# Optimization experiments

Measured on AMD Instinct MI355X. Metric: run time of the kernel, lower is better.

Reference implementation:

```python
import jax, jax.numpy as jnp
import numpy as np

N = 100000

def _gcn_conv(x, W, b, row, col, norm, n_nodes):
    # x: [N, Fin], W: [Fin, Fout]; message = norm * (x W)[row], aggregated at col
    h = x @ W                                  # small GEMM
    msg = h[row] * norm[:, None]               # [E+N, Fout] gather (memory bound)
    out = jax.ops.segment_sum(msg, col, num_segments=n_nodes)
    return out + b

def _norm_coeffs(edge_index, n_nodes):
    # add self-loops, compute symmetric normalization deg^-1/2[row]*deg^-1/2[col]
    loops = jnp.arange(n_nodes, dtype=edge_index.dtype)
    row = jnp.concatenate([edge_index[0], loops])
    col = jnp.concatenate([edge_index[1], loops])
    deg = jax.ops.segment_sum(jnp.ones_like(col, dtype=jnp.float32), col,
                              num_segments=n_nodes)
    dinv = jnp.where(deg > 0, jax.lax.rsqrt(deg), 0.0)
    norm = dinv[row] * dinv[col]
    return row, col, norm

def setup_inputs() -> dict:
    key = jax.random.key(0)
    ks = jax.random.split(key, 4)
    x = jax.random.normal(ks[0], (N, 64), dtype=jnp.float32)
    edge_index = jax.random.randint(ks[1], (2, 1600000), 0, N, dtype=jnp.int64)
    W1 = jax.random.normal(ks[2], (64, 64), dtype=jnp.float32) / np.sqrt(64)
    b1 = jnp.zeros((64,), dtype=jnp.float32)
    W2 = jax.random.normal(ks[3], (64, 64), dtype=jnp.float32) / np.sqrt(64)
    b2 = jnp.zeros((64,), dtype=jnp.float32)
    return {"x": x, "edge_index": edge_index, "W1": W1, "b1": b1, "W2": W2, "b2": b2}

def reference(x, edge_index, W1, b1, W2, b2):
    row, col, norm = _norm_coeffs(edge_index, N)
    h = jax.nn.relu(_gcn_conv(x, W1, b1, row, col, norm, N))
    return _gcn_conv(h, W2, b2, row, col, norm, N)
```

## Files before the change

### kernel.cpp

```cpp
#include <hip/hip_runtime.h>


#define NPB 32
#define BSH 8
#define BSZ 256
#define PTILE 4096
#define CAP 6144
#define PADALLOW 3856
#define CROW (CAP + PADALLOW)

typedef __attribute__((ext_vector_type(8))) short bf16x8;
typedef __attribute__((ext_vector_type(4))) float f32x4;

__device__ __forceinline__ unsigned bf16_rne(float f) {
    unsigned b = __float_as_uint(f);
    return (b + 0x7fffu + ((b >> 16) & 1u)) >> 16;
}
__device__ __forceinline__ float bf16_lo(unsigned u) { return __uint_as_float(u << 16); }
__device__ __forceinline__ float bf16_hi(unsigned u) { return __uint_as_float(u & 0xffff0000u); }

__global__ __launch_bounds__(512) void k_count(const int* __restrict__ coli,
                                               int E, int N, int NB, int numTiles,
                                               int* __restrict__ tcnt) {
    __shared__ int hist[512];
    int t = threadIdx.x;
    int T = E + N;
    int tile = blockIdx.x;
    int tstart = tile * PTILE;
    int m = min(PTILE, T - tstart);
    for (int b = t; b < NB; b += 512) hist[b] = 0;
    __syncthreads();
    for (int i = t; i < m; i += 512) {
        int g = tstart + i;
        int c = (g < E) ? coli[g] : (g - E);
        atomicAdd(&hist[c >> BSH], 1);
    }
    __syncthreads();
    for (int b = t; b < NB; b += 512) tcnt[(size_t)tile * NB + b] = hist[b];
}

__global__ __launch_bounds__(512) void k_scan(int* __restrict__ tcnt,
                                              int* __restrict__ btot,
                                              int NB, int numTiles) {
    __shared__ int wsum[8];
    int b = blockIdx.x;
    int t = threadIdx.x;
    int lane = t & 63, wid = t >> 6;
    int base = 0;
    for (int c0 = 0; c0 < numTiles; c0 += 512) {
        int tt = c0 + t;
        int v = (tt < numTiles) ? tcnt[(size_t)tt * NB + b] : 0;
        int inc = v;
        #pragma unroll
        for (int d = 1; d < 64; d <<= 1) {
            int o = __shfl_up(inc, d);
            if (lane >= d) inc += o;
        }
        if (lane == 63) wsum[wid] = inc;
        __syncthreads();
        int woff = 0, ctot = 0;
        #pragma unroll
        for (int i = 0; i < 8; i++) {
            int s = wsum[i];
            if (i < wid) woff += s;
            ctot += s;
        }
        if (tt < numTiles) tcnt[(size_t)tt * NB + b] = b * CAP + base + woff + inc - v;
        base += ctot;
        __syncthreads();
    }
    if (t == 0) btot[b] = base;
}

__global__ __launch_bounds__(512) void k_scatter(const int* __restrict__ rowi,
                                                 const int* __restrict__ coli,
                                                 int E, int N, int NB, int numTiles,
                                                 const int* __restrict__ tcnt,
                                                 unsigned* __restrict__ pairs) {
    __shared__ int hist[512];
    __shared__ int lbase[512];
    __shared__ int gbase[512];
    __shared__ unsigned sorted[PTILE];
    __shared__ unsigned short sbkt[PTILE];
    __shared__ int wsum[8];
    int t = threadIdx.x;
    int T = E + N;
    int tile = blockIdx.x;
    int tstart = tile * PTILE;
    int m = min(PTILE, T - tstart);
    for (int b = t; b < NB; b += 512) {
        hist[b] = 0;
        gbase[b] = tcnt[(size_t)tile * NB + b];
    }
    __syncthreads();
    int c_reg[8];
    #pragma unroll
    for (int k = 0; k < 8; k++) {
        int i = t + k * 512;
        int c = 0;
        if (i < m) {
            int g = tstart + i;
            c = (g < E) ? coli[g] : (g - E);
            atomicAdd(&hist[c >> BSH], 1);
        }
        c_reg[k] = c;
    }
    __syncthreads();
    {
        int lane = t & 63, wid = t >> 6;
        int v = (t < NB) ? hist[t] : 0;
        int inc = v;
        #pragma unroll
        for (int d = 1; d < 64; d <<= 1) {
            int o = __shfl_up(inc, d);
            if (lane >= d) inc += o;
        }
        if (lane == 63) wsum[wid] = inc;
        __syncthreads();
        int woff = 0;
        for (int i = 0; i < wid; i++) woff += wsum[i];
        if (t < NB) lbase[t] = woff + inc - v;
        __syncthreads();
    }
    for (int b = t; b < NB; b += 512) hist[b] = 0;
    __syncthreads();
    #pragma unroll
    for (int k = 0; k < 8; k++) {
        int i = t + k * 512;
        if (i < m) {
            int g = tstart + i;
            int c = c_reg[k];
            int r = (g < E) ? rowi[g] : c;
            int b = c >> BSH;
            int lr = atomicAdd(&hist[b], 1);
            int pos = lbase[b] + lr;
            sorted[pos] = (unsigned)r | ((unsigned)(c & (BSZ - 1)) << 24);
            sbkt[pos] = (unsigned short)b;
        }
    }
    __syncthreads();
    for (int j = t; j < m; j += 512) {
        int b = sbkt[j];
        pairs[gbase[b] + (j - lbase[b])] = sorted[j];
    }
}

__global__ __launch_bounds__(1024) void k_bfill(const unsigned* __restrict__ pairs,
                                                const int* __restrict__ btot,
                                                int N,
                                                int* __restrict__ offsets,
                                                int* __restrict__ cnt,
                                                float* __restrict__ dinv,
                                                int* __restrict__ csrc) {
    __shared__ int scnt[BSZ];
    __shared__ int scur[BSZ];
    __shared__ int wsum[4];
    __shared__ int scsrc[CROW];
    int b = blockIdx.x;
    int t = threadIdx.x;
    int ebeg = b * CAP;
    int m = btot[b];
    int pbase = b * CROW;
    if (t < BSZ) scnt[t] = 0;
    __syncthreads();
    for (int i = t; i < m; i += 1024) {
        atomicAdd(&scnt[pairs[ebeg + i] >> 24], 1);
    }
    __syncthreads();
    int cval = 0, pc = 0, inc = 0;
    int lane = t & 63, wid = t >> 6;
    if (t < BSZ) {
        cval = scnt[t];
        pc = (cval + 15) & ~15;
        inc = pc;
        #pragma unroll
        for (int d = 1; d < 64; d <<= 1) {
            int o = __shfl_up(inc, d);
            if (lane >= d) inc += o;
        }
        if (lane == 63) wsum[wid] = inc;
    }
    __syncthreads();
    if (t < BSZ) {
        int woff = 0;
        for (int i = 0; i < wid; i++) woff += wsum[i];
        int offl = woff + inc - pc;
        int v = (b << BSH) + t;
        if (v < N) {
            offsets[v] = pbase + offl;
            cnt[v] = (cval + 1) & ~1;
            dinv[v] = rsqrtf((float)cval);
        }
        scur[t] = offl;
        for (int i = offl + cval; i < offl + pc; i++) scsrc[i] = N;
    }
    __syncthreads();
    for (int i = t; i < m; i += 1024) {
        unsigned pk = pairs[ebeg + i];
        int slot = atomicAdd(&scur[pk >> 24], 1);
        scsrc[slot] = (int)(pk & 0xFFFFFFu);
    }
    __syncthreads();
    int tot = wsum[0] + wsum[1] + wsum[2] + wsum[3];
    for (int j = t; j < tot; j += 1024) csrc[pbase + j] = scsrc[j];
}

template <bool BF16IN>
__global__ __launch_bounds__(256) void k_gemm(const void* __restrict__ Xv,
                                              const float* __restrict__ W,
                                              const float* __restrict__ dinv,
                                              unsigned* __restrict__ Hout,
                                              int N, int nSlabs, int slabStride) {
    __shared__ float SMEM[4224];
    int t = threadIdx.x;
    int lane = t & 63, w = t >> 6;
    int nn = lane & 15, kq = lane >> 4;

    for (int i = t; i < 1024; i += 256) ((float4*)SMEM)[i] = ((const float4*)W)[i];
    __syncthreads();
    bf16x8 Bf[2][4];
    #pragma unroll
    for (int kt = 0; kt < 2; kt++) {
        #pragma unroll
        for (int ct = 0; ct < 4; ct++) {
            union { bf16x8 v; unsigned short s[8]; } u;
            #pragma unroll
            for (int j = 0; j < 8; j++) {
                int k = kt * 32 + kq * 8 + j;
                u.s[j] = (unsigned short)bf16_rne(SMEM[k * 64 + ct * 16 + nn]);
            }
            Bf[kt][ct] = u.v;
        }
    }
    __syncthreads();

    float* outT = SMEM + w * 1056;

    for (int slab = blockIdx.x * 4 + w; slab < nSlabs; slab += slabStride) {
        int row0 = slab * 16;
        int rowA = min(row0 + nn, N - 1);
        bf16x8 A0, A1;
        if (BF16IN) {
            const uint4* X = (const uint4*)Xv;
            union { uint4 u; bf16x8 v; } a0, a1;
            a0.u = X[(size_t)rowA * 8 + kq];
            a1.u = X[(size_t)rowA * 8 + 4 + kq];
            A0 = a0.v; A1 = a1.v;
        } else {
            const float4* X = (const float4*)Xv;
            float4 f0 = X[(size_t)rowA * 16 + kq * 2];
            float4 f1 = X[(size_t)rowA * 16 + kq * 2 + 1];
            float4 f2 = X[(size_t)rowA * 16 + 8 + kq * 2];
            float4 f3 = X[(size_t)rowA * 16 + 8 + kq * 2 + 1];
            union { bf16x8 v; unsigned short s[8]; } a0, a1;
            a0.s[0] = (unsigned short)bf16_rne(f0.x); a0.s[1] = (unsigned short)bf16_rne(f0.y);
            a0.s[2] = (unsigned short)bf16_rne(f0.z); a0.s[3] = (unsigned short)bf16_rne(f0.w);
            a0.s[4] = (unsigned short)bf16_rne(f1.x); a0.s[5] = (unsigned short)bf16_rne(f1.y);
            a0.s[6] = (unsigned short)bf16_rne(f1.z); a0.s[7] = (unsigned short)bf16_rne(f1.w);
            a1.s[0] = (unsigned short)bf16_rne(f2.x); a1.s[1] = (unsigned short)bf16_rne(f2.y);
            a1.s[2] = (unsigned short)bf16_rne(f2.z); a1.s[3] = (unsigned short)bf16_rne(f2.w);
            a1.s[4] = (unsigned short)bf16_rne(f3.x); a1.s[5] = (unsigned short)bf16_rne(f3.y);
            a1.s[6] = (unsigned short)bf16_rne(f3.z); a1.s[7] = (unsigned short)bf16_rne(f3.w);
            A0 = a0.v; A1 = a1.v;
        }
        float dvm = dinv[rowA];

        f32x4 acc[4];
        #pragma unroll
        for (int ct = 0; ct < 4; ct++) acc[ct] = (f32x4){0.f, 0.f, 0.f, 0.f};
        #pragma unroll
        for (int ct = 0; ct < 4; ct++) {
            acc[ct] = __builtin_amdgcn_mfma_f32_16x16x32_bf16(A0, Bf[0][ct], acc[ct], 0, 0, 0);
            acc[ct] = __builtin_amdgcn_mfma_f32_16x16x32_bf16(A1, Bf[1][ct], acc[ct], 0, 0, 0);
        }

        #pragma unroll
        for (int reg = 0; reg < 4; reg++) {
            int r = kq * 4 + reg;
            float dv = __shfl(dvm, r);
            #pragma unroll
            for (int ct = 0; ct < 4; ct++) {
                outT[r * 66 + ct * 16 + nn] = acc[ct][reg] * dv;
            }
        }
        int rr = lane >> 2;
        int c0 = (lane & 3) * 16;
        int orow = row0 + rr;
        if (orow < N) {
            unsigned pk[8];
            #pragma unroll
            for (int i = 0; i < 8; i++) {
                float lo = outT[rr * 66 + c0 + 2 * i];
                float hi = outT[rr * 66 + c0 + 2 * i + 1];
                pk[i] = bf16_rne(lo) | (bf16_rne(hi) << 16);
            }
            uint4* dst = (uint4*)Hout + (size_t)orow * 8 + (lane & 3) * 2;
            dst[0] = make_uint4(pk[0], pk[1], pk[2], pk[3]);
            dst[1] = make_uint4(pk[4], pk[5], pk[6], pk[7]);
        } else if (orow == N) {
            uint4* dst = (uint4*)Hout + (size_t)N * 8 + (lane & 3) * 2;
            dst[0] = make_uint4(0, 0, 0, 0);
            dst[1] = make_uint4(0, 0, 0, 0);
        }
    }
}

template <bool RELU_BF16OUT>
__global__ __launch_bounds__(256) void k_agg(const uint4* __restrict__ H,
                                             const int* __restrict__ offsets,
                                             const int* __restrict__ cnt,
                                             const int* __restrict__ csrc,
                                             const float* __restrict__ dinv,
                                             const float* __restrict__ bias,
                                             void* __restrict__ outv, int N) {
    int t = threadIdx.x;
    int fl = t & 7;
    int v = blockIdx.x * NPB + (t >> 3);
    if (v >= N) return;
    int beg = offsets[v];
    int deg = cnt[v];
    const int2* cs2 = (const int2*)(csrc + beg);
    const char* hb = (const char*)H + ((unsigned)fl << 4);

    float a0 = 0.f, a1 = 0.f, a2 = 0.f, a3 = 0.f;
    float a4 = 0.f, a5 = 0.f, a6 = 0.f, a7 = 0.f;

#define ACC8(R) do {                                                        \
        uint4 dd = *(const uint4*)(hb + ((unsigned)(R) << 7));              \
        a0 += bf16_lo(dd.x); a1 += bf16_hi(dd.x);                           \
        a2 += bf16_lo(dd.y); a3 += bf16_hi(dd.y);                           \
        a4 += bf16_lo(dd.z); a5 += bf16_hi(dd.z);                           \
        a6 += bf16_lo(dd.w); a7 += bf16_hi(dd.w);                           \
    } while (0)

    int2 ss = cs2[0];
    for (int j = 2; j < deg; j += 2) {
        int2 nx = cs2[j >> 1];
        ACC8(ss.x);
        ACC8(ss.y);
        ss = nx;
    }
    ACC8(ss.x);
    ACC8(ss.y);
#undef ACC8

    float dv = dinv[v];
    const float4* b4 = (const float4*)bias;
    float4 bA = b4[fl * 2];
    float4 bB = b4[fl * 2 + 1];
    float r0 = fmaf(dv, a0, bA.x);
    float r1 = fmaf(dv, a1, bA.y);
    float r2 = fmaf(dv, a2, bA.z);
    float r3 = fmaf(dv, a3, bA.w);
    float r4 = fmaf(dv, a4, bB.x);
    float r5 = fmaf(dv, a5, bB.y);
    float r6 = fmaf(dv, a6, bB.z);
    float r7 = fmaf(dv, a7, bB.w);
    if (RELU_BF16OUT) {
        r0 = fmaxf(r0, 0.f); r1 = fmaxf(r1, 0.f);
        r2 = fmaxf(r2, 0.f); r3 = fmaxf(r3, 0.f);
        r4 = fmaxf(r4, 0.f); r5 = fmaxf(r5, 0.f);
        r6 = fmaxf(r6, 0.f); r7 = fmaxf(r7, 0.f);
        uint4 pk;
        pk.x = bf16_rne(r0) | (bf16_rne(r1) << 16);
        pk.y = bf16_rne(r2) | (bf16_rne(r3) << 16);
        pk.z = bf16_rne(r4) | (bf16_rne(r5) << 16);
        pk.w = bf16_rne(r6) | (bf16_rne(r7) << 16);
        ((uint4*)outv)[(size_t)v * 8 + fl] = pk;
    } else {
        float4* o = (float4*)outv + (size_t)v * 16 + fl * 2;
        o[0] = make_float4(r0, r1, r2, r3);
        o[1] = make_float4(r4, r5, r6, r7);
    }
}

extern "C" void kernel_launch(void* const* d_in, const int* in_sizes, int n_in,
                              void* d_out, int out_size, void* d_ws, size_t ws_size,
                              hipStream_t stream) {
    const float* x  = (const float*)d_in[0];
    const int*   ei = (const int*)d_in[1];
    const float* W1 = (const float*)d_in[2];
    const float* b1 = (const float*)d_in[3];
    const float* W2 = (const float*)d_in[4];
    const float* b2 = (const float*)d_in[5];
    float* out      = (float*)d_out;

    const int N = in_sizes[0] / 64;
    const int E = in_sizes[1] / 2;
    const int* row = ei;
    const int* col = ei + E;
    const int T = E + N;
    const int NB = (N + BSZ - 1) >> BSH;
    const int numTiles = (T + PTILE - 1) / PTILE;

    char* p = (char*)d_ws;
    auto alloc = [&](size_t bytes) { void* r = (void*)p; p += (bytes + 255) & ~(size_t)255; return r; };
    int*      tcnt    = (int*)alloc((size_t)NB * numTiles * 4);
    int*      btot    = (int*)alloc((size_t)(NB + 1) * 4);
    int*      offsets = (int*)alloc((size_t)N * 4);
    int*      cnt     = (int*)alloc((size_t)N * 4);
    float*    dinv    = (float*)alloc((size_t)N * 4);
    unsigned* pairs   = (unsigned*)alloc((size_t)NB * CAP * 4);
    int*      csrc    = (int*)alloc(((size_t)NB * CROW + 64) * 4);
    unsigned* hbuf    = (unsigned*)alloc((size_t)(N + 16) * 32 * 4);
    unsigned* abuf    = (unsigned*)alloc((size_t)(N + 16) * 32 * 4);

    k_count<<<numTiles, 512, 0, stream>>>(col, E, N, NB, numTiles, tcnt);
    k_scan<<<NB, 512, 0, stream>>>(tcnt, btot, NB, numTiles);
    k_scatter<<<numTiles, 512, 0, stream>>>(row, col, E, N, NB, numTiles, tcnt, pairs);
    k_bfill<<<NB, 1024, 0, stream>>>(pairs, btot, N, offsets, cnt, dinv, csrc);

    const int nSlabs = (N + 16) / 16;
    const int GEMM_BLOCKS = 1024;
    const int SLAB_STRIDE = GEMM_BLOCKS * 4;
    const int GB = (N + NPB - 1) / NPB;

    k_gemm<false><<<GEMM_BLOCKS, 256, 0, stream>>>(x, W1, dinv, hbuf, N, nSlabs, SLAB_STRIDE);
    k_agg<true><<<GB, 256, 0, stream>>>((const uint4*)hbuf, offsets, cnt, csrc, dinv, b1, abuf, N);
    k_gemm<true><<<GEMM_BLOCKS, 256, 0, stream>>>(abuf, W2, dinv, hbuf, N, nSlabs, SLAB_STRIDE);
    k_agg<false><<<GB, 256, 0, stream>>>((const uint4*)hbuf, offsets, cnt, csrc, dinv, b2, out, N);
}
```

Before: 198.0 us.

## Fuse first GEMM into count kernel and apply source dinv during aggregation

Takes the dinv source scaling out of the GEMM epilogue, so the first-layer GEMM no longer waits for degree computation. That GEMM now runs as extra blocks inside the edge-count kernel, overlapping with the histogram pass and removing one launch. In exchange, the aggregation loop gathers dinv[src] per edge and uses FMAs, adding extra scattered loads on the memory-bound gather path. The GEMM is also executed with 512-thread blocks within the fused launch.

```diff
diff --git a/kernel.cpp b/kernel.cpp
--- a/kernel.cpp
+++ b/kernel.cpp
@@ -8,6 +8,7 @@
 #define CAP 6144
 #define PADALLOW 3856
 #define CROW (CAP + PADALLOW)
+#define GEMMB 1024
 
 typedef __attribute__((ext_vector_type(8))) short bf16x8;
 typedef __attribute__((ext_vector_type(4))) float f32x4;
@@ -19,204 +20,18 @@
 __device__ __forceinline__ float bf16_lo(unsigned u) { return __uint_as_float(u << 16); }
 __device__ __forceinline__ float bf16_hi(unsigned u) { return __uint_as_float(u & 0xffff0000u); }
 
-__global__ __launch_bounds__(512) void k_count(const int* __restrict__ coli,
-                                               int E, int N, int NB, int numTiles,
-                                               int* __restrict__ tcnt) {
-    __shared__ int hist[512];
-    int t = threadIdx.x;
-    int T = E + N;
-    int tile = blockIdx.x;
-    int tstart = tile * PTILE;
-    int m = min(PTILE, T - tstart);
-    for (int b = t; b < NB; b += 512) hist[b] = 0;
-    __syncthreads();
-    for (int i = t; i < m; i += 512) {
-        int g = tstart + i;
-        int c = (g < E) ? coli[g] : (g - E);
-        atomicAdd(&hist[c >> BSH], 1);
-    }
-    __syncthreads();
-    for (int b = t; b < NB; b += 512) tcnt[(size_t)tile * NB + b] = hist[b];
-}
-
-__global__ __launch_bounds__(512) void k_scan(int* __restrict__ tcnt,
-                                              int* __restrict__ btot,
-                                              int NB, int numTiles) {
-    __shared__ int wsum[8];
-    int b = blockIdx.x;
-    int t = threadIdx.x;
-    int lane = t & 63, wid = t >> 6;
-    int base = 0;
-    for (int c0 = 0; c0 < numTiles; c0 += 512) {
-        int tt = c0 + t;
-        int v = (tt < numTiles) ? tcnt[(size_t)tt * NB + b] : 0;
-        int inc = v;
-        #pragma unroll
-        for (int d = 1; d < 64; d <<= 1) {
-            int o = __shfl_up(inc, d);
-            if (lane >= d) inc += o;
-        }
-        if (lane == 63) wsum[wid] = inc;
-        __syncthreads();
-        int woff = 0, ctot = 0;
-        #pragma unroll
-        for (int i = 0; i < 8; i++) {
-            int s = wsum[i];
-            if (i < wid) woff += s;
-            ctot += s;
-        }
-        if (tt < numTiles) tcnt[(size_t)tt * NB + b] = b * CAP + base + woff + inc - v;
-        base += ctot;
-        __syncthreads();
-    }
-    if (t == 0) btot[b] = base;
-}
-
-__global__ __launch_bounds__(512) void k_scatter(const int* __restrict__ rowi,
-                                                 const int* __restrict__ coli,
-                                                 int E, int N, int NB, int numTiles,
-                                                 const int* __restrict__ tcnt,
-                                                 unsigned* __restrict__ pairs) {
-    __shared__ int hist[512];
-    __shared__ int lbase[512];
-    __shared__ int gbase[512];
-    __shared__ unsigned sorted[PTILE];
-    __shared__ unsigned short sbkt[PTILE];
-    __shared__ int wsum[8];
-    int t = threadIdx.x;
-    int T = E + N;
-    int tile = blockIdx.x;
-    int tstart = tile * PTILE;
-    int m = min(PTILE, T - tstart);
-    for (int b = t; b < NB; b += 512) {
-        hist[b] = 0;
-        gbase[b] = tcnt[(size_t)tile * NB + b];
-    }
-    __syncthreads();
-    int c_reg[8];
-    #pragma unroll
-    for (int k = 0; k < 8; k++) {
-        int i = t + k * 512;
-        int c = 0;
-        if (i < m) {
-            int g = tstart + i;
-            c = (g < E) ? coli[g] : (g - E);
-            atomicAdd(&hist[c >> BSH], 1);
-        }
-        c_reg[k] = c;
-    }
-    __syncthreads();
-    {
-        int lane = t & 63, wid = t >> 6;
-        int v = (t < NB) ? hist[t] : 0;
-        int inc = v;
-        #pragma unroll
-        for (int d = 1; d < 64; d <<= 1) {
-            int o = __shfl_up(inc, d);
-            if (lane >= d) inc += o;
-        }
-        if (lane == 63) wsum[wid] = inc;
-        __syncthreads();
-        int woff = 0;
-        for (int i = 0; i < wid; i++) woff += wsum[i];
-        if (t < NB) lbase[t] = woff + inc - v;
-        __syncthreads();
-    }
-    for (int b = t; b < NB; b += 512) hist[b] = 0;
-    __syncthreads();
-    #pragma unroll
-    for (int k = 0; k < 8; k++) {
-        int i = t + k * 512;
-        if (i < m) {
-            int g = tstart + i;
-            int c = c_reg[k];
-            int r = (g < E) ? rowi[g] : c;
-            int b = c >> BSH;
-            int lr = atomicAdd(&hist[b], 1);
-            int pos = lbase[b] + lr;
-            sorted[pos] = (unsigned)r | ((unsigned)(c & (BSZ - 1)) << 24);
-            sbkt[pos] = (unsigned short)b;
-        }
-    }
-    __syncthreads();
-    for (int j = t; j < m; j += 512) {
-        int b = sbkt[j];
-        pairs[gbase[b] + (j - lbase[b])] = sorted[j];
-    }
-}
-
-__global__ __launch_bounds__(1024) void k_bfill(const unsigned* __restrict__ pairs,
-                                                const int* __restrict__ btot,
-                                                int N,
-                                                int* __restrict__ offsets,
-                                                int* __restrict__ cnt,
-                                                float* __restrict__ dinv,
-                                                int* __restrict__ csrc) {
-    __shared__ int scnt[BSZ];
-    __shared__ int scur[BSZ];
-    __shared__ int wsum[4];
-    __shared__ int scsrc[CROW];
-    int b = blockIdx.x;
-    int t = threadIdx.x;
-    int ebeg = b * CAP;
-    int m = btot[b];
-    int pbase = b * CROW;
-    if (t < BSZ) scnt[t] = 0;
-    __syncthreads();
-    for (int i = t; i < m; i += 1024) {
-        atomicAdd(&scnt[pairs[ebeg + i] >> 24], 1);
-    }
-    __syncthreads();
-    int cval = 0, pc = 0, inc = 0;
-    int lane = t & 63, wid = t >> 6;
-    if (t < BSZ) {
-        cval = scnt[t];
-        pc = (cval + 15) & ~15;
-        inc = pc;
-        #pragma unroll
-        for (int d = 1; d < 64; d <<= 1) {
-            int o = __shfl_up(inc, d);
-            if (lane >= d) inc += o;
-        }
-        if (lane == 63) wsum[wid] = inc;
-    }
-    __syncthreads();
-    if (t < BSZ) {
-        int woff = 0;
-        for (int i = 0; i < wid; i++) woff += wsum[i];
-        int offl = woff + inc - pc;
-        int v = (b << BSH) + t;
-        if (v < N) {
-            offsets[v] = pbase + offl;
-            cnt[v] = (cval + 1) & ~1;
-            dinv[v] = rsqrtf((float)cval);
-        }
-        scur[t] = offl;
-        for (int i = offl + cval; i < offl + pc; i++) scsrc[i] = N;
-    }
-    __syncthreads();
-    for (int i = t; i < m; i += 1024) {
-        unsigned pk = pairs[ebeg + i];
-        int slot = atomicAdd(&scur[pk >> 24], 1);
-        scsrc[slot] = (int)(pk & 0xFFFFFFu);
-    }
-    __syncthreads();
-    int tot = wsum[0] + wsum[1] + wsum[2] + wsum[3];
-    for (int j = t; j < tot; j += 1024) csrc[pbase + j] = scsrc[j];
-}
-
-template <bool BF16IN>
-__global__ __launch_bounds__(256) void k_gemm(const void* __restrict__ Xv,
-                                              const float* __restrict__ W,
-                                              const float* __restrict__ dinv,
-                                              unsigned* __restrict__ Hout,
-                                              int N, int nSlabs, int slabStride) {
-    __shared__ float SMEM[4224];
+template <bool BF16IN, int NT>
+__device__ __forceinline__ void gemm_body(const void* __restrict__ Xv,
+                                          const float* __restrict__ W,
+                                          unsigned* __restrict__ Hout,
+                                          int N, int nSlabs, int blkLocal,
+                                          int nBlkLocal, float* SMEM) {
     int t = threadIdx.x;
     int lane = t & 63, w = t >> 6;
     int nn = lane & 15, kq = lane >> 4;
-
-    for (int i = t; i < 1024; i += 256) ((float4*)SMEM)[i] = ((const float4*)W)[i];
+    constexpr int NW = NT / 64;
+
+    for (int i = t; i < 1024; i += NT) ((float4*)SMEM)[i] = ((const float4*)W)[i];
     __syncthreads();
     bf16x8 Bf[2][4];
     #pragma unroll
@@ -236,7 +51,7 @@
 
     float* outT = SMEM + w * 1056;
 
-    for (int slab = blockIdx.x * 4 + w; slab < nSlabs; slab += slabStride) {
+    for (int slab = blkLocal * NW + w; slab < nSlabs; slab += nBlkLocal * NW) {
         int row0 = slab * 16;
         int rowA = min(row0 + nn, N - 1);
         bf16x8 A0, A1;
@@ -263,7 +78,6 @@
             a1.s[6] = (unsigned short)bf16_rne(f3.z); a1.s[7] = (unsigned short)bf16_rne(f3.w);
             A0 = a0.v; A1 = a1.v;
         }
-        float dvm = dinv[rowA];
 
         f32x4 acc[4];
         #pragma unroll
@@ -277,10 +91,9 @@
         #pragma unroll
         for (int reg = 0; reg < 4; reg++) {
             int r = kq * 4 + reg;
-            float dv = __shfl(dvm, r);
             #pragma unroll
             for (int ct = 0; ct < 4; ct++) {
-                outT[r * 66 + ct * 16 + nn] = acc[ct][reg] * dv;
+                outT[r * 66 + ct * 16 + nn] = acc[ct][reg];
             }
         }
         int rr = lane >> 2;
@@ -305,6 +118,209 @@
     }
 }
 
+__global__ __launch_bounds__(512) void k_cntgm(const int* __restrict__ coli,
+                                               int E, int N, int NB, int numTiles,
+                                               int* __restrict__ tcnt,
+                                               const float* __restrict__ x,
+                                               const float* __restrict__ W1,
+                                               unsigned* __restrict__ hbuf,
+                                               int nSlabs) {
+    __shared__ float SMEM[8448];
+    int bid = blockIdx.x;
+    if (bid >= numTiles) {
+        gemm_body<false, 512>(x, W1, hbuf, N, nSlabs, bid - numTiles, GEMMB, SMEM);
+        return;
+    }
+    int* hist = (int*)SMEM;
+    int t = threadIdx.x;
+    int T = E + N;
+    int tstart = bid * PTILE;
+    int m = min(PTILE, T - tstart);
+    for (int b = t; b < NB; b += 512) hist[b] = 0;
+    __syncthreads();
+    for (int i = t; i < m; i += 512) {
+        int g = tstart + i;
+        int c = (g < E) ? coli[g] : (g - E);
+        atomicAdd(&hist[c >> BSH], 1);
+    }
+    __syncthreads();
+    for (int b = t; b < NB; b += 512) tcnt[(size_t)bid * NB + b] = hist[b];
+}
+
+__global__ __launch_bounds__(512) void k_scan(int* __restrict__ tcnt,
+                                              int* __restrict__ btot,
+                                              int NB, int numTiles) {
+    __shared__ int wsum[8];
+    int b = blockIdx.x;
+    int t = threadIdx.x;
+    int lane = t & 63, wid = t >> 6;
+    int base = 0;
+    for (int c0 = 0; c0 < numTiles; c0 += 512) {
+        int tt = c0 + t;
+        int v = (tt < numTiles) ? tcnt[(size_t)tt * NB + b] : 0;
+        int inc = v;
+        #pragma unroll
+        for (int d = 1; d < 64; d <<= 1) {
+            int o = __shfl_up(inc, d);
+            if (lane >= d) inc += o;
+        }
+        if (lane == 63) wsum[wid] = inc;
+        __syncthreads();
+        int woff = 0, ctot = 0;
+        #pragma unroll
+        for (int i = 0; i < 8; i++) {
+            int s = wsum[i];
+            if (i < wid) woff += s;
+            ctot += s;
+        }
+        if (tt < numTiles) tcnt[(size_t)tt * NB + b] = b * CAP + base + woff + inc - v;
+        base += ctot;
+        __syncthreads();
+    }
+    if (t == 0) btot[b] = base;
+}
+
+__global__ __launch_bounds__(512) void k_scatter(const int* __restrict__ rowi,
+                                                 const int* __restrict__ coli,
+                                                 int E, int N, int NB, int numTiles,
+                                                 const int* __restrict__ tcnt,
+                                                 unsigned* __restrict__ pairs) {
+    __shared__ int hist[512];
+    __shared__ int lbase[512];
+    __shared__ int gbase[512];
+    __shared__ unsigned sorted[PTILE];
+    __shared__ unsigned short sbkt[PTILE];
+    __shared__ int wsum[8];
+    int t = threadIdx.x;
+    int T = E + N;
+    int tile = blockIdx.x;
+    int tstart = tile * PTILE;
+    int m = min(PTILE, T - tstart);
+    int lane = t & 63, wid = t >> 6;
+    for (int b = t; b < NB; b += 512) {
+        hist[b] = 0;
+        gbase[b] = tcnt[(size_t)tile * NB + b];
+    }
+    __syncthreads();
+    int c_reg[8];
+    #pragma unroll
+    for (int k = 0; k < 8; k++) {
+        int i = t + k * 512;
+        int c = 0;
+        if (i < m) {
+            int g = tstart + i;
+            c = (g < E) ? coli[g] : (g - E);
+            atomicAdd(&hist[c >> BSH], 1);
+        }
+        c_reg[k] = c;
+    }
+    __syncthreads();
+    {
+        int v = (t < NB) ? hist[t] : 0;
+        int inc = v;
+        #pragma unroll
+        for (int d = 1; d < 64; d <<= 1) {
+            int o = __shfl_up(inc, d);
+            if (lane >= d) inc += o;
+        }
+        if (lane == 63) wsum[wid] = inc;
+        __syncthreads();
+        int woff = 0;
+        for (int i = 0; i < wid; i++) woff += wsum[i];
+        if (t < NB) lbase[t] = woff + inc - v;
+        __syncthreads();
+    }
+    for (int b = t; b < NB; b += 512) hist[b] = 0;
+    __syncthreads();
+    #pragma unroll
+    for (int k = 0; k < 8; k++) {
+        int i = t + k * 512;
+        if (i < m) {
+            int g = tstart + i;
+            int c = c_reg[k];
+            int r = (g < E) ? rowi[g] : c;
+            int b = c >> BSH;
+            int lr = atomicAdd(&hist[b], 1);
+            int pos = lbase[b] + lr;
+            sorted[pos] = (unsigned)r | ((unsigned)(c & (BSZ - 1)) << 24);
+            sbkt[pos] = (unsigned short)b;
+        }
+    }
+    __syncthreads();
+    for (int j = t; j < m; j += 512) {
+        int b = sbkt[j];
+        pairs[gbase[b] + (j - lbase[b])] = sorted[j];
+    }
+}
+
+__global__ __launch_bounds__(1024) void k_bfill(const unsigned* __restrict__ pairs,
+                                                const int* __restrict__ btot,
+                                                int N,
+                                                int* __restrict__ offsets,
+                                                int* __restrict__ cnt,
+                                                float* __restrict__ dinv,
+                                                int* __restrict__ csrc) {
+    __shared__ int scnt[BSZ];
+    __shared__ int scur[BSZ];
+    __shared__ int wsum[4];
+    __shared__ int scsrc[CROW];
+    int b = blockIdx.x;
+    int t = threadIdx.x;
+    int ebeg = b * CAP;
+    int m = btot[b];
+    int pbase = b * CROW;
+    int lane = t & 63, wid = t >> 6;
+    if (b == 0 && t == 0) dinv[N] = 0.0f;
+    if (t < BSZ) scnt[t] = 0;
+    __syncthreads();
+    for (int i = t; i < m; i += 1024) atomicAdd(&scnt[pairs[ebeg + i] >> 24], 1);
+    __syncthreads();
+    int cval = 0, pc = 0, inc = 0;
+    if (t < BSZ) {
+        cval = scnt[t];
+        pc = (cval + 15) & ~15;
+        inc = pc;
+        #pragma unroll
+        for (int d = 1; d < 64; d <<= 1) {
+            int o = __shfl_up(inc, d);
+            if (lane >= d) inc += o;
+        }
+        if (lane == 63) wsum[wid] = inc;
+    }
+    __syncthreads();
+    if (t < BSZ) {
+        int woff = 0;
+        for (int i = 0; i < wid; i++) woff += wsum[i];
+        int offl = woff + inc - pc;
+        int v = (b << BSH) + t;
+        if (v < N) {
+            offsets[v] = pbase + offl;
+            cnt[v] = (cval + 1) & ~1;
+            dinv[v] = rsqrtf((float)cval);
+        }
+        scur[t] = offl;
+        for (int i = offl + cval; i < offl + pc; i++) scsrc[i] = N;
+    }
+    __syncthreads();
+    for (int i = t; i < m; i += 1024) {
+        unsigned pk = pairs[ebeg + i];
+        int slot = atomicAdd(&scur[pk >> 24], 1);
+        scsrc[slot] = (int)(pk & 0xFFFFFFu);
+    }
+    __syncthreads();
+    int tot = wsum[0] + wsum[1] + wsum[2] + wsum[3];
+    for (int j = t; j < tot; j += 1024) csrc[pbase + j] = scsrc[j];
+}
+
+template <bool BF16IN>
+__global__ __launch_bounds__(256) void k_gemm(const void* __restrict__ Xv,
+                                              const float* __restrict__ W,
+                                              unsigned* __restrict__ Hout,
+                                              int N, int nSlabs, int nBlk) {
+    __shared__ float SMEM[4224];
+    gemm_body<BF16IN, 256>(Xv, W, Hout, N, nSlabs, blockIdx.x, nBlk, SMEM);
+}
+
 template <bool RELU_BF16OUT>
 __global__ __launch_bounds__(256) void k_agg(const uint4* __restrict__ H,
                                              const int* __restrict__ offsets,
@@ -325,23 +341,25 @@
     float a0 = 0.f, a1 = 0.f, a2 = 0.f, a3 = 0.f;
     float a4 = 0.f, a5 = 0.f, a6 = 0.f, a7 = 0.f;
 
-#define ACC8(R) do {                                                        \
+#define ACC8(R, D) do {                                                     \
         uint4 dd = *(const uint4*)(hb + ((unsigned)(R) << 7));              \
-        a0 += bf16_lo(dd.x); a1 += bf16_hi(dd.x);                           \
-        a2 += bf16_lo(dd.y); a3 += bf16_hi(dd.y);                           \
-        a4 += bf16_lo(dd.z); a5 += bf16_hi(dd.z);                           \
-        a6 += bf16_lo(dd.w); a7 += bf16_hi(dd.w);                           \
+        a0 = fmaf(D, bf16_lo(dd.x), a0); a1 = fmaf(D, bf16_hi(dd.x), a1);   \
+        a2 = fmaf(D, bf16_lo(dd.y), a2); a3 = fmaf(D, bf16_hi(dd.y), a3);   \
+        a4 = fmaf(D, bf16_lo(dd.z), a4); a5 = fmaf(D, bf16_hi(dd.z), a5);   \
+        a6 = fmaf(D, bf16_lo(dd.w), a6); a7 = fmaf(D, bf16_hi(dd.w), a7);   \
     } while (0)
 
     int2 ss = cs2[0];
+    float dsx = dinv[ss.x], dsy = dinv[ss.y];
     for (int j = 2; j < deg; j += 2) {
         int2 nx = cs2[j >> 1];
-        ACC8(ss.x);
-        ACC8(ss.y);
-        ss = nx;
-    }
-    ACC8(ss.x);
-    ACC8(ss.y);
+        float dnx = dinv[nx.x], dny = dinv[nx.y];
+        ACC8(ss.x, dsx);
+        ACC8(ss.y, dsy);
+        ss = nx; dsx = dnx; dsy = dny;
+    }
+    ACC8(ss.x, dsx);
+    ACC8(ss.y, dsy);
 #undef ACC8
 
     float dv = dinv[v];
@@ -399,24 +417,22 @@
     int*      btot    = (int*)alloc((size_t)(NB + 1) * 4);
     int*      offsets = (int*)alloc((size_t)N * 4);
     int*      cnt     = (int*)alloc((size_t)N * 4);
-    float*    dinv    = (float*)alloc((size_t)N * 4);
+    float*    dinv    = (float*)alloc((size_t)(N + 16) * 4);
     unsigned* pairs   = (unsigned*)alloc((size_t)NB * CAP * 4);
     int*      csrc    = (int*)alloc(((size_t)NB * CROW + 64) * 4);
     unsigned* hbuf    = (unsigned*)alloc((size_t)(N + 16) * 32 * 4);
     unsigned* abuf    = (unsigned*)alloc((size_t)(N + 16) * 32 * 4);
 
-    k_count<<<numTiles, 512, 0, stream>>>(col, E, N, NB, numTiles, tcnt);
+    const int nSlabs = (N + 16) / 16;
+    const int GB = (N + NPB - 1) / NPB;
+
+    k_cntgm<<<numTiles + GEMMB, 512, 0, stream>>>(col, E, N, NB, numTiles, tcnt,
+                                                  x, W1, hbuf, nSlabs);
     k_scan<<<NB, 512, 0, stream>>>(tcnt, btot, NB, numTiles);
     k_scatter<<<numTiles, 512, 0, stream>>>(row, col, E, N, NB, numTiles, tcnt, pairs);
     k_bfill<<<NB, 1024, 0, stream>>>(pairs, btot, N, offsets, cnt, dinv, csrc);
 
-    const int nSlabs = (N + 16) / 16;
-    const int GEMM_BLOCKS = 1024;
-    const int SLAB_STRIDE = GEMM_BLOCKS * 4;
-    const int GB = (N + NPB - 1) / NPB;
-
-    k_gemm<false><<<GEMM_BLOCKS, 256, 0, stream>>>(x, W1, dinv, hbuf, N, nSlabs, SLAB_STRIDE);
     k_agg<true><<<GB, 256, 0, stream>>>((const uint4*)hbuf, offsets, cnt, csrc, dinv, b1, abuf, N);
-    k_gemm<true><<<GEMM_BLOCKS, 256, 0, stream>>>(abuf, W2, dinv, hbuf, N, nSlabs, SLAB_STRIDE);
+    k_gemm<true><<<1024, 256, 0, stream>>>(abuf, W2, hbuf, N, nSlabs, 1024);
     k_agg<false><<<GB, 256, 0, stream>>>((const uint4*)hbuf, offsets, cnt, csrc, dinv, b2, out, N);
 }
```

Result: no change. 200.2 us (+1.1%).
